# Optimization experiments

Hardware: AMD Instinct MI355X
Metric: run time of the kernel (lower is better)

Reference implementation:

```python
import jax, jax.numpy as jnp
import numpy as np

NDIR = 6  # build_tree.num_directions()

def prelu(x, alpha):
    return jnp.where(x >= 0, x, alpha * x)

def setup_inputs() -> dict:
    key = jax.random.key(0)
    ks = jax.random.split(key, 8)
    B, N_IN, N_OUT, IDIM, ODIM, V = 16, 16384, 8192, 128, 128, 64
    last = jax.random.normal(ks[0], (B, N_IN, IDIM), dtype=jnp.float32)
    vec = jax.random.randint(ks[1], (B, N_OUT), 0, V)
    dmap = jax.random.randint(ks[2], (V,), 0, NDIR)
    drev = jax.random.randint(ks[3], (V,), 0, 2)
    child_l = jax.random.randint(ks[4], (N_OUT,), 0, N_IN)
    child_r = jax.random.randint(ks[5], (N_OUT,), 0, N_IN)
    # stacked per-direction Linear(idim*2, odim) weights/biases
    W = jax.random.normal(ks[6], (NDIR, 2 * IDIM, ODIM), dtype=jnp.float32) * (1.0 / np.sqrt(2 * IDIM))
    b = jax.random.normal(ks[7], (NDIR, ODIM), dtype=jnp.float32) * 0.01
    alpha = jnp.array(0.005, dtype=jnp.float32)  # PReLU init weight
    return {"last": last, "W": W, "b": b, "alpha": alpha, "vec": vec,
            "dmap": dmap, "drev": drev, "child_l": child_l, "child_r": child_r}

def reference(last, W, b, alpha, vec, dmap, drev, child_l, child_r):
    # gather per-edge direction-reverse flag: [B, N_OUT, 1]
    r = drev[vec].astype(last.dtype)[:, :, None]
    lch = last[:, child_l]  # [B, N_OUT, IDIM]
    rch = last[:, child_r]  # [B, N_OUT, IDIM]
    # direction-masked child swap, concat -> [B, N_OUT, 2*IDIM]
    pair = jnp.concatenate([lch * (1 - r) + rch * r,
                            rch * (1 - r) + lch * r], axis=-1)
    dirs = dmap[vec][:, :, None]  # direction id per node, [B, N_OUT, 1]
    ndir = W.shape[0]
    tmp = jnp.zeros(pair.shape[:2] + (W.shape[-1],), dtype=last.dtype)
    # masked grouped GEMM: each node routed to its direction's Linear
    for i in range(ndir):  # small fixed set of relation types
        y = pair @ W[i] + b[i]
        tmp = tmp + jnp.where(dirs == i, y, jnp.zeros((), dtype=last.dtype))
    return prelu(tmp, alpha)
```

## Files before the change

### kernel.cpp

```cpp
#include <hip/hip_runtime.h>

#define NDIR  6
#define B_    16
#define N_IN  16384
#define N_OUT 8192
#define IDIM  128
#define ODIM  128
#define TOTAL (B_ * N_OUT)
#define BM    64
#define MAXBLK (TOTAL / BM + NDIR)

#define WS_CNT 0
#define WS_OFF 8
#define WS_CUR 16
#define WS_BLK 24
#define WS_IDS 64
#define WS_WT  131584

using s16x8 = __attribute__((ext_vector_type(8))) short;
using f32x4 = __attribute__((ext_vector_type(4))) float;

__global__ void zero_kernel(int* ws) {
    int t = threadIdx.x;
    if (t < 32) ws[t] = 0;
}

__global__ void count_kernel(const int* __restrict__ vec, const int* __restrict__ dmap,
                             int* __restrict__ ws) {
    __shared__ int h[NDIR];
    int t = threadIdx.x;
    if (t < NDIR) h[t] = 0;
    __syncthreads();
    int id = blockIdx.x * 256 + t;
    if (id < TOTAL) {
        int d = dmap[vec[id]];
        atomicAdd(&h[d], 1);
    }
    __syncthreads();
    if (t < NDIR && h[t]) atomicAdd(&ws[WS_CNT + t], h[t]);
}

__global__ void prefix_kernel(int* ws) {
    if (threadIdx.x == 0) {
        int acc = 0, bacc = 0;
        for (int i = 0; i < NDIR; ++i) {
            ws[WS_OFF + i] = acc;
            ws[WS_CUR + i] = acc;
            ws[WS_BLK + i] = bacc;
            int c = ws[WS_CNT + i];
            acc += c;
            bacc += (c + BM - 1) / BM;
        }
        ws[WS_OFF + NDIR] = acc;
        ws[WS_BLK + NDIR] = bacc;
    }
}

__global__ void scatter_kernel(const int* __restrict__ vec, const int* __restrict__ dmap,
                               int* __restrict__ ws) {
    __shared__ int h[NDIR];
    __shared__ int base[NDIR];
    int t = threadIdx.x;
    if (t < NDIR) h[t] = 0;
    __syncthreads();
    int id = blockIdx.x * 256 + t;
    int d = 0, pos = 0;
    if (id < TOTAL) {
        d = dmap[vec[id]];
        pos = atomicAdd(&h[d], 1);
    }
    __syncthreads();
    if (t < NDIR) base[t] = h[t] ? atomicAdd(&ws[WS_CUR + t], h[t]) : 0;
    __syncthreads();
    if (id < TOTAL) ws[WS_IDS + base[d] + pos] = id;
}

__global__ void wconvert_kernel(const float* __restrict__ W, int* __restrict__ ws) {
    unsigned short* wt = (unsigned short*)(ws + WS_WT);
    int g = blockIdx.x * 256 + threadIdx.x;
    int dsb = g >> 12;
    int e = g & 4095;
    int col = e >> 5;
    int kk = e & 31;
    int cp = kk >> 3, i = kk & 7;
    int key = (col >> 1) & 3;
    int d = dsb >> 3, s = dsb & 7;
    int ksrc = s * 32 + ((cp ^ key) << 3) + i;
    float w = W[((d * 256) + ksrc) * 128 + col];
    unsigned u = __float_as_uint(w);
    float hf = __uint_as_float(u & 0xFFFF0000u);
    float lf = w - hf;
    int base = dsb * 8192 + col * 32 + cp * 8 + i;
    wt[base] = (unsigned short)(u >> 16);
    wt[base + 4096] = (unsigned short)(__float_as_uint(lf) >> 16);
}

__device__ __forceinline__ void cvt8(float4 a, float4 b, s16x8& h, s16x8& lo) {
    float x[8] = {a.x, a.y, a.z, a.w, b.x, b.y, b.z, b.w};
    #pragma unroll
    for (int j = 0; j < 8; ++j) {
        unsigned u = __float_as_uint(x[j]);
        float hf = __uint_as_float(u & 0xFFFF0000u);
        float lf = x[j] - hf;
        h[j] = (short)(u >> 16);
        lo[j] = (short)(__float_as_uint(lf) >> 16);
    }
}

#define CFENCE() asm volatile("" ::: "memory")

__global__ __launch_bounds__(256, 3) void gemm_kernel(
    const float* __restrict__ last, const float* __restrict__ bias,
    const float* __restrict__ alphap,
    const int* __restrict__ vec, const int* __restrict__ drev,
    const int* __restrict__ child_l, const int* __restrict__ child_r,
    const int* __restrict__ ws, float* __restrict__ out)
{
    int i = blockIdx.x;
    if (i >= ws[WS_BLK + NDIR]) return;
    int dir = 0;
    #pragma unroll
    for (int d = 1; d < NDIR; ++d)
        if (i >= ws[WS_BLK + d]) dir = d;
    int tile = i - ws[WS_BLK + dir];
    int start = ws[WS_OFF + dir];
    int end   = ws[WS_OFF + dir + 1];
    int m0 = start + tile * BM;
    const int* ids = ws + WS_IDS;

    __shared__ unsigned short wbuf[2][8192];
    __shared__ int s_row0[BM], s_row1[BM], s_oid[BM];

    int t = threadIdx.x;
    int l = t & 63;
    int wid = t >> 6;

    if (t < BM) {
        int idx = m0 + t;
        bool valid = idx < end;
        int id = ids[valid ? idx : end - 1];
        int b = id >> 13;
        int n = id & (N_OUT - 1);
        int v = vec[id];
        int r = drev[v];
        int cl = child_l[n];
        int cr = child_r[n];
        int first  = r ? cr : cl;
        int second = r ? cl : cr;
        s_row0[t] = b * N_IN + first;
        s_row1[t] = b * N_IN + second;
        s_oid[t]  = valid ? id : -1;
    }
    __syncthreads();

    int m = wid * 16 + (l & 15);
    int rowA[2] = { s_row0[m], s_row1[m] };

    const char* wt_blk = (const char*)(ws + WS_WT) + (size_t)dir * 8 * 16384;

    #define STAGE_W(buf, s_)                                                     \
        {                                                                        \
            const char* gsrc = wt_blk + (size_t)(s_) * 16384 + wid * 4096 + l * 16; \
            char* ldst = (char*)&wbuf[buf][0] + wid * 4096;                      \
            _Pragma("unroll")                                                    \
            for (int i_ = 0; i_ < 4; ++i_) {                                     \
                __builtin_amdgcn_global_load_lds(                                \
                    (const __attribute__((address_space(1))) void*)(gsrc + i_ * 1024), \
                    (__attribute__((address_space(3))) void*)(ldst + i_ * 1024), \
                    16, 0, 0);                                                   \
            }                                                                    \
        }

    #define ISSUE_R(arr, h_)                                                     \
        {                                                                        \
            const float* rbase = last + (size_t)rowA[h_] * IDIM + (l >> 4) * 8;  \
            _Pragma("unroll")                                                    \
            for (int c_ = 0; c_ < 4; ++c_) {                                     \
                arr[c_ * 2]     = *(const float4*)(rbase + c_ * 32);             \
                arr[c_ * 2 + 1] = *(const float4*)(rbase + c_ * 32 + 4);         \
            }                                                                    \
        }

    f32x4 acc[8];
    #pragma unroll
    for (int nf = 0; nf < 8; ++nf)
        acc[nf] = (f32x4){0.f, 0.f, 0.f, 0.f};

    float4 xaA[8], xaB[8];

    STAGE_W(0, 0);
    CFENCE();
    ISSUE_R(xaA, 0);
    CFENCE();

    #pragma unroll
    for (int s = 0; s < 8; ++s) {
        int cur = s & 1;
        if (s < 7) { STAGE_W(cur ^ 1, s + 1); CFENCE(); }
        if (s == 1)      { asm volatile("s_waitcnt vmcnt(12)" ::: "memory"); }
        else if (s == 7) { asm volatile("s_waitcnt vmcnt(0)"  ::: "memory"); }
        else             { asm volatile("s_waitcnt vmcnt(4)"  ::: "memory"); }
        __builtin_amdgcn_s_barrier();
        CFENCE();
        s16x8 ah, al;
        if (s < 4) cvt8(xaA[(s & 3) * 2], xaA[(s & 3) * 2 + 1], ah, al);
        else       cvt8(xaB[(s & 3) * 2], xaB[(s & 3) * 2 + 1], ah, al);
        if (s == 0) { CFENCE(); ISSUE_R(xaB, 1); CFENCE(); }
        #pragma unroll
        for (int q = 0; q < 4; ++q) {
            s16x8 bh[2], bl[2];
            #pragma unroll
            for (int i2 = 0; i2 < 2; ++i2) {
                int nf = q * 2 + i2;
                int col = nf * 16 + (l & 15);
                int cp = (l >> 4) ^ ((col >> 1) & 3);
                int off = col * 32 + cp * 8;
                bh[i2] = *(const s16x8*)&wbuf[cur][off];
                bl[i2] = *(const s16x8*)&wbuf[cur][off + 4096];
            }
            #pragma unroll
            for (int i2 = 0; i2 < 2; ++i2) {
                int nf = q * 2 + i2;
                acc[nf] = __builtin_amdgcn_mfma_f32_16x16x32_bf16(ah, bh[i2], acc[nf], 0, 0, 0);
                acc[nf] = __builtin_amdgcn_mfma_f32_16x16x32_bf16(ah, bl[i2], acc[nf], 0, 0, 0);
                acc[nf] = __builtin_amdgcn_mfma_f32_16x16x32_bf16(al, bh[i2], acc[nf], 0, 0, 0);
            }
        }
        if (s < 7) {
            CFENCE();
            __builtin_amdgcn_s_barrier();
            CFENCE();
        }
    }

    float alpha = alphap[0];
    #pragma unroll
    for (int nf = 0; nf < 8; ++nf) {
        int col = nf * 16 + (l & 15);
        float bv = bias[dir * ODIM + col];
        #pragma unroll
        for (int j = 0; j < 4; ++j) {
            int mloc = wid * 16 + (l >> 4) * 4 + j;
            int id = s_oid[mloc];
            if (id < 0) continue;
            float y = acc[nf][j] + bv;
            out[(size_t)id * ODIM + col] = y >= 0.f ? y : alpha * y;
        }
    }
    #undef STAGE_W
    #undef ISSUE_R
}

extern "C" void kernel_launch(void* const* d_in, const int* in_sizes, int n_in,
                              void* d_out, int out_size, void* d_ws, size_t ws_size,
                              hipStream_t stream) {
    const float* last    = (const float*)d_in[0];
    const float* W       = (const float*)d_in[1];
    const float* bias    = (const float*)d_in[2];
    const float* alpha   = (const float*)d_in[3];
    const int*   vec     = (const int*)d_in[4];
    const int*   dmap    = (const int*)d_in[5];
    const int*   drev    = (const int*)d_in[6];
    const int*   child_l = (const int*)d_in[7];
    const int*   child_r = (const int*)d_in[8];
    float* out = (float*)d_out;
    int*   ws  = (int*)d_ws;

    zero_kernel<<<1, 64, 0, stream>>>(ws);
    count_kernel<<<TOTAL / 256, 256, 0, stream>>>(vec, dmap, ws);
    prefix_kernel<<<1, 64, 0, stream>>>(ws);
    scatter_kernel<<<TOTAL / 256, 256, 0, stream>>>(vec, dmap, ws);
    wconvert_kernel<<<(NDIR * 8 * 4096) / 256, 256, 0, stream>>>(W, ws);
    gemm_kernel<<<MAXBLK, 256, 0, stream>>>(last, bias, alpha, vec, drev,
                                            child_l, child_r, ws, out);
}
```

Measured before the change: 88.51 us.

## Bucket node ordering by direction and source-row region to improve gather locality

```diff
diff --git a/kernel.cpp b/kernel.cpp
--- a/kernel.cpp
+++ b/kernel.cpp
@@ -9,70 +9,102 @@
 #define TOTAL (B_ * N_OUT)
 #define BM    64
 #define MAXBLK (TOTAL / BM + NDIR)
-
-#define WS_CNT 0
-#define WS_OFF 8
-#define WS_CUR 16
-#define WS_BLK 24
-#define WS_IDS 64
-#define WS_WT  131584
+#define NBUCKET 128
+#define NKEY (NDIR * NBUCKET)
+
+#define WS_OFF  8
+#define WS_BLK  24
+#define WS_CNT2 64
+#define WS_CURS 2048
+#define WS_IDS  4096
+#define WS_WT   135168
 
 using s16x8 = __attribute__((ext_vector_type(8))) short;
 using f32x4 = __attribute__((ext_vector_type(4))) float;
 
+__device__ __forceinline__ int node_key(const int* vec, const int* dmap,
+                                        const int* drev, const int* child_l,
+                                        const int* child_r, int id, int* dirOut) {
+    int v = vec[id];
+    int d = dmap[v];
+    int r = drev[v];
+    int n = id & (N_OUT - 1);
+    int b = id >> 13;
+    int first = r ? child_r[n] : child_l[n];
+    *dirOut = d;
+    return d * NBUCKET + ((b * N_IN + first) >> 11);
+}
+
 __global__ void zero_kernel(int* ws) {
     int t = threadIdx.x;
-    if (t < 32) ws[t] = 0;
+    for (int k = t; k < NKEY; k += 256) ws[WS_CNT2 + k] = 0;
 }
 
 __global__ void count_kernel(const int* __restrict__ vec, const int* __restrict__ dmap,
-                             int* __restrict__ ws) {
-    __shared__ int h[NDIR];
-    int t = threadIdx.x;
-    if (t < NDIR) h[t] = 0;
+                             const int* __restrict__ drev, const int* __restrict__ child_l,
+                             const int* __restrict__ child_r, int* __restrict__ ws) {
+    __shared__ int h[NKEY];
+    int t = threadIdx.x;
+    for (int k = t; k < NKEY; k += 256) h[k] = 0;
     __syncthreads();
     int id = blockIdx.x * 256 + t;
-    if (id < TOTAL) {
-        int d = dmap[vec[id]];
-        atomicAdd(&h[d], 1);
-    }
-    __syncthreads();
-    if (t < NDIR && h[t]) atomicAdd(&ws[WS_CNT + t], h[t]);
+    int dir;
+    int key = node_key(vec, dmap, drev, child_l, child_r, id, &dir);
+    atomicAdd(&h[key], 1);
+    __syncthreads();
+    for (int k = t; k < NKEY; k += 256)
+        if (h[k]) atomicAdd(&ws[WS_CNT2 + k], h[k]);
 }
 
 __global__ void prefix_kernel(int* ws) {
-    if (threadIdx.x == 0) {
-        int acc = 0, bacc = 0;
-        for (int i = 0; i < NDIR; ++i) {
-            ws[WS_OFF + i] = acc;
-            ws[WS_CUR + i] = acc;
-            ws[WS_BLK + i] = bacc;
-            int c = ws[WS_CNT + i];
-            acc += c;
-            bacc += (c + BM - 1) / BM;
-        }
-        ws[WS_OFF + NDIR] = acc;
+    __shared__ int part[256];
+    __shared__ int ex[256];
+    int t = threadIdx.x;
+    int c[3], s = 0;
+    #pragma unroll
+    for (int j = 0; j < 3; ++j) { c[j] = ws[WS_CNT2 + t * 3 + j]; s += c[j]; }
+    part[t] = s;
+    __syncthreads();
+    if (t == 0) {
+        int a = 0;
+        for (int i = 0; i < 256; ++i) { ex[i] = a; a += part[i]; }
+    }
+    __syncthreads();
+    int a = ex[t];
+    #pragma unroll
+    for (int j = 0; j < 3; ++j) { ws[WS_CURS + t * 3 + j] = a; a += c[j]; }
+    __threadfence();
+    __syncthreads();
+    if (t == 0) {
+        for (int d = 0; d < NDIR; ++d) ws[WS_OFF + d] = ws[WS_CURS + d * NBUCKET];
+        ws[WS_OFF + NDIR] = TOTAL;
+        int bacc = 0;
+        for (int d = 0; d < NDIR; ++d) {
+            ws[WS_BLK + d] = bacc;
+            int cnt = ws[WS_OFF + d + 1] - ws[WS_OFF + d];
+            bacc += (cnt + BM - 1) / BM;
+        }
         ws[WS_BLK + NDIR] = bacc;
     }
 }
 
 __global__ void scatter_kernel(const int* __restrict__ vec, const int* __restrict__ dmap,
-                               int* __restrict__ ws) {
-    __shared__ int h[NDIR];
-    __shared__ int base[NDIR];
-    int t = threadIdx.x;
-    if (t < NDIR) h[t] = 0;
+                               const int* __restrict__ drev, const int* __restrict__ child_l,
+                               const int* __restrict__ child_r, int* __restrict__ ws) {
+    __shared__ int h[NKEY];
+    __shared__ int base[NKEY];
+    int t = threadIdx.x;
+    for (int k = t; k < NKEY; k += 256) h[k] = 0;
     __syncthreads();
     int id = blockIdx.x * 256 + t;
-    int d = 0, pos = 0;
-    if (id < TOTAL) {
-        d = dmap[vec[id]];
-        pos = atomicAdd(&h[d], 1);
-    }
-    __syncthreads();
-    if (t < NDIR) base[t] = h[t] ? atomicAdd(&ws[WS_CUR + t], h[t]) : 0;
-    __syncthreads();
-    if (id < TOTAL) ws[WS_IDS + base[d] + pos] = id;
+    int dir;
+    int key = node_key(vec, dmap, drev, child_l, child_r, id, &dir);
+    int pos = atomicAdd(&h[key], 1);
+    __syncthreads();
+    for (int k = t; k < NKEY; k += 256)
+        base[k] = h[k] ? atomicAdd(&ws[WS_CURS + k], h[k]) : 0;
+    __syncthreads();
+    ws[WS_IDS + base[key] + pos] = id;
 }
 
 __global__ void wconvert_kernel(const float* __restrict__ W, int* __restrict__ ws) {
@@ -266,10 +298,10 @@
     float* out = (float*)d_out;
     int*   ws  = (int*)d_ws;
 
-    zero_kernel<<<1, 64, 0, stream>>>(ws);
-    count_kernel<<<TOTAL / 256, 256, 0, stream>>>(vec, dmap, ws);
-    prefix_kernel<<<1, 64, 0, stream>>>(ws);
-    scatter_kernel<<<TOTAL / 256, 256, 0, stream>>>(vec, dmap, ws);
+    zero_kernel<<<1, 256, 0, stream>>>(ws);
+    count_kernel<<<TOTAL / 256, 256, 0, stream>>>(vec, dmap, drev, child_l, child_r, ws);
+    prefix_kernel<<<1, 256, 0, stream>>>(ws);
+    scatter_kernel<<<TOTAL / 256, 256, 0, stream>>>(vec, dmap, drev, child_l, child_r, ws);
     wconvert_kernel<<<(NDIR * 8 * 4096) / 256, 256, 0, stream>>>(W, ws);
     gemm_kernel<<<MAXBLK, 256, 0, stream>>>(last, bias, alpha, vec, drev,
                                             child_l, child_r, ws, out);
```

After: 83.87 us. -5.2%, faster.
